# Performance work log

Measured on AMD Instinct MI355X. Metric: run time of the kernel, lower is better.

The kernel has to match this reference:

```python
import jax, jax.numpy as jnp
import numpy as np


def setup_inputs() -> dict:
    key = jax.random.key(0)
    ks = jax.random.split(key, 12)
    B, T, N, H = 32, 128, 256, 512
    s = 0.05
    return {
        "data": jax.random.normal(ks[0], (B, T, N), jnp.float32),
        "h0": jax.random.normal(ks[1], (B, H), jnp.float32),
        "gru_kernel": jax.random.normal(ks[2], (N, 3 * H), jnp.float32) * s,
        "gru_rkernel": jax.random.normal(ks[3], (H, 3 * H), jnp.float32) * s,
        "gru_bias": jax.random.normal(ks[4], (2, 3 * H), jnp.float32) * s,  # (input_bias, recurrent_bias), reset_after=True
        "w1_w": jax.random.normal(ks[5], (T, T), jnp.float32) * s,
        "w1_b": jax.random.normal(ks[6], (T,), jnp.float32) * s,
        "w2_w": jax.random.normal(ks[7], (H, T), jnp.float32) * s,
        "w2_b": jax.random.normal(ks[8], (T,), jnp.float32) * s,
        "v_w": jax.random.normal(ks[9], (T, 1), jnp.float32) * s,
        "v_b": jax.random.normal(ks[10], (1,), jnp.float32) * s,
        "n": N,
    }


def reference(data, h0, gru_kernel, gru_rkernel, gru_bias, w1_w, w1_b, w2_w, w2_b, v_w, v_b, n):
    B, T, N = data.shape
    b_in, b_rec = gru_bias[0], gru_bias[1]

    # Keras GRUCell (reset_after=True, gate order z,r,h)
    def step(h, x_t):
        mx = x_t @ gru_kernel + b_in          # (B,3H)
        mh = h @ gru_rkernel + b_rec          # (B,3H)
        xz, xr, xh = jnp.split(mx, 3, axis=-1)
        hz, hr, hh = jnp.split(mh, 3, axis=-1)
        z = jax.nn.sigmoid(xz + hz)
        r = jax.nn.sigmoid(xr + hr)
        c = jnp.tanh(xh + r * hh)
        h_new = z * h + (1.0 - z) * c
        return h_new, h_new

    xs = jnp.swapaxes(data, 0, 1)                               # (T,B,N)
    _, hs = jax.lax.scan(step, h0, xs)                          # (T,B,H) hidden state after each step

    # Input attention, vectorized over t (attention does not feed back into the GRU)
    x_perm = jnp.swapaxes(data, 1, 2)                           # (B,N,T)
    score_x = jnp.einsum('bnt,tu->bnu', x_perm, w1_w) + w1_b    # (B,N,T), constant across steps
    h_proj = hs @ w2_w + w2_b                                   # (T,B,T)
    e = jnp.tanh(score_x[None, :, :, :] + h_proj[:, :, None, :])  # (T,B,N,T)
    score = jnp.einsum('tbnu,u->tbn', e, v_w[:, 0]) + v_b[0]    # (T,B,N)
    alpha = jax.nn.softmax(score, axis=-1)                      # (T,B,N) softmax over features

    # Replicates tf.reshape(alpha_seq.stack(), (-1, T, n)) on (T,B,1,N) (row-major)
    alpha_seq = alpha.reshape(-1, T, N)                         # (B,T,N) via flat reindex, as in original
    return data * alpha_seq
```

## Files before the change

### kernel.cpp

```cpp
#include <hip/hip_runtime.h>
#include <math.h>

#define BB 32
#define TT 128
#define NF 256
#define HH 512
#define G3 1536
#define NWG 64

__device__ __forceinline__ float sigmoidf_(float x) { return 1.f / (1.f + __expf(-x)); }
__device__ __forceinline__ float tanh_fast(float x) {
    float e = __expf(2.f * x);
    return 1.f - 2.f / (e + 1.f);
}
__device__ __forceinline__ float sel4_(float a0, float a1, float a2, float a3, int s) {
    float s01 = (s & 1) ? a1 : a0;
    float s23 = (s & 1) ? a3 : a2;
    return (s & 2) ? s23 : s01;
}

__global__ __launch_bounds__(256) void k_hinit(const float* __restrict__ h0,
                                               float* __restrict__ hg2) {
    int idx = blockIdx.x * 256 + threadIdx.x;
    int i = idx & 511, b = idx >> 9;
    hg2[i * BB + b] = h0[b * HH + i];
}

__global__ __launch_bounds__(256) void k_pack(const float* __restrict__ rk,
                                              float4* __restrict__ rk4) {
    int gidx = blockIdx.x * 256 + threadIdx.x;
    int wg = gidx >> 12;
    int idx = gidx & 4095;
    int k = idx >> 3, s = idx & 7;
    int jjL = s ^ (((k >> 7) & 3) << 1);
    const float* r = rk + (size_t)k * G3 + wg * 8 + jjL;
    rk4[gidx] = make_float4(r[0], r[512], r[1024], 0.f);
}

__global__ __launch_bounds__(256) void k_mx(const float* __restrict__ data,
                                            const float* __restrict__ gk,
                                            const float* __restrict__ bias_in,
                                            float* __restrict__ mx) {
    __shared__ __align__(16) float xs[NF * 8];
    int bx = blockIdx.x;
    int t = bx >> 2, b0 = (bx & 3) * 8;
    int tid = threadIdx.x;
    for (int idx = tid; idx < 8 * NF; idx += 256) {
        int bb = idx >> 8, k = idx & 255;
        xs[k * 8 + bb] = data[((size_t)(b0 + bb) * TT + t) * NF + k];
    }
    __syncthreads();
    float acc[6][8];
#pragma unroll
    for (int jj = 0; jj < 6; jj++)
#pragma unroll
        for (int bb = 0; bb < 8; bb++) acc[jj][bb] = 0.f;

    for (int k = 0; k < NF; k++) {
        float4 xa = *(const float4*)&xs[k * 8];
        float4 xb = *(const float4*)&xs[k * 8 + 4];
        float xv[8] = {xa.x, xa.y, xa.z, xa.w, xb.x, xb.y, xb.z, xb.w};
#pragma unroll
        for (int jj = 0; jj < 6; jj++) {
            float g = gk[(size_t)k * G3 + jj * 256 + tid];
#pragma unroll
            for (int bb = 0; bb < 8; bb++) acc[jj][bb] += g * xv[bb];
        }
    }
#pragma unroll
    for (int jj = 0; jj < 6; jj++) {
        int j = jj * 256 + tid;
        float bi = bias_in[j];
#pragma unroll
        for (int bb = 0; bb < 8; bb++)
            mx[((size_t)t * BB + b0 + bb) * G3 + j] = acc[jj][bb] + bi;
    }
}

extern __shared__ float4 wl4_dyn[];

__global__ __launch_bounds__(256, 1) void k_gstep(const float4* __restrict__ rk4,
                                                  const float* __restrict__ gbias,
                                                  const float* __restrict__ mx,
                                                  float* __restrict__ hg2,
                                                  float* __restrict__ hs,
                                                  int t) {
    __shared__ __align__(16) float4 h4[HH * 8];
    const int tid = threadIdx.x;
    const int wg  = blockIdx.x;
    const int jj  = tid >> 5;
    const int bq  = (tid >> 2) & 7;
    const int ks  = tid & 3;
    const int i0  = wg * 8;
    const int i   = i0 + jj;
    const int batch = bq * 4 + ks;
    const int jjs = jj ^ (ks << 1);
    const int bqs = bq ^ (ks << 1);

    {
        const float4* src = rk4 + (size_t)wg * 4096;
#pragma unroll
        for (int it = 0; it < 16; it++) {
            int idx = it * 256 + tid;
            wl4_dyn[idx] = src[idx];
        }
    }
    {
        const float4* hgr = (const float4*)(hg2 + (t & 1) * (HH * BB));
#pragma unroll
        for (int it = 0; it < 16; it++) {
            int idx = it * 256 + tid;
            h4[idx] = hgr[idx ^ ((((idx >> 10) & 3)) << 1)];
        }
    }
    const float* brec = gbias + G3;
    const float bz = brec[i], br_ = brec[512 + i], bh = brec[1024 + i];
    __syncthreads();

    const float* mxr = mx + ((size_t)t * BB + batch) * G3;
    float mz = mxr[i], mr = mxr[512 + i], mh = mxr[1024 + i];

    float az0 = 0.f, az1 = 0.f, az2 = 0.f, az3 = 0.f;
    float ar0 = 0.f, ar1 = 0.f, ar2 = 0.f, ar3 = 0.f;
    float ah0 = 0.f, ah1 = 0.f, ah2 = 0.f, ah3 = 0.f;
    const float4* wp  = wl4_dyn + ks * 1024 + jjs;
    const float4* hp2 = &h4[ks * 1024 + bqs];
#pragma unroll 4
    for (int kk = 0; kk < 128; kk++) {
        float4 w = wp[kk * 8];
        float4 h = hp2[kk * 8];
        az0 += w.x * h.x; az1 += w.x * h.y; az2 += w.x * h.z; az3 += w.x * h.w;
        ar0 += w.y * h.x; ar1 += w.y * h.y; ar2 += w.y * h.z; ar3 += w.y * h.w;
        ah0 += w.z * h.x; ah1 += w.z * h.y; ah2 += w.z * h.z; ah3 += w.z * h.w;
    }

    az0 += __shfl_xor(az0, 1); az1 += __shfl_xor(az1, 1);
    az2 += __shfl_xor(az2, 1); az3 += __shfl_xor(az3, 1);
    ar0 += __shfl_xor(ar0, 1); ar1 += __shfl_xor(ar1, 1);
    ar2 += __shfl_xor(ar2, 1); ar3 += __shfl_xor(ar3, 1);
    ah0 += __shfl_xor(ah0, 1); ah1 += __shfl_xor(ah1, 1);
    ah2 += __shfl_xor(ah2, 1); ah3 += __shfl_xor(ah3, 1);
    az0 += __shfl_xor(az0, 2); az1 += __shfl_xor(az1, 2);
    az2 += __shfl_xor(az2, 2); az3 += __shfl_xor(az3, 2);
    ar0 += __shfl_xor(ar0, 2); ar1 += __shfl_xor(ar1, 2);
    ar2 += __shfl_xor(ar2, 2); ar3 += __shfl_xor(ar3, 2);
    ah0 += __shfl_xor(ah0, 2); ah1 += __shfl_xor(ah1, 2);
    ah2 += __shfl_xor(ah2, 2); ah3 += __shfl_xor(ah3, 2);

    float azt = sel4_(az0, az1, az2, az3, ks);
    float art = sel4_(ar0, ar1, ar2, ar3, ks);
    float aht = sel4_(ah0, ah1, ah2, ah3, ks);

    float z = sigmoidf_(mz + azt + bz);
    float r = sigmoidf_(mr + art + br_);
    float c = tanhf(mh + r * (aht + bh));
    float hold = ((const float*)&h4[i * 8 + (bq ^ ((((i >> 7) & 3)) << 1))])[ks];
    float hn = z * hold + (1.f - z) * c;

    hg2[((t + 1) & 1) * (HH * BB) + i * BB + batch] = hn;
    hs[((size_t)t * BB + batch) * HH + i] = hn;
}

__global__ __launch_bounds__(256) void k_sx(const float* __restrict__ data,
                                            const float* __restrict__ w1,
                                            const float* __restrict__ w1b,
                                            float* __restrict__ sx) {
    int bx = blockIdx.x;
    int b = bx >> 4, ug = bx & 15;
    int n = threadIdx.x;
    float acc[8] = {0, 0, 0, 0, 0, 0, 0, 0};
    const float* dp = data + (size_t)b * TT * NF + n;
    for (int t = 0; t < TT; t++) {
        float x = dp[(size_t)t * NF];
#pragma unroll
        for (int uu = 0; uu < 8; uu++) acc[uu] += x * w1[t * TT + ug * 8 + uu];
    }
#pragma unroll
    for (int uu = 0; uu < 8; uu++) {
        int u = ug * 8 + uu;
        sx[((size_t)b * TT + u) * NF + n] = acc[uu] + w1b[u];
    }
}

__global__ __launch_bounds__(256) void k_hp(const float* __restrict__ hs,
                                            const float* __restrict__ w2,
                                            const float* __restrict__ w2b,
                                            float* __restrict__ hp) {
    __shared__ float hsl[8 * HH];
    int r0 = blockIdx.x * 8;
    int tid = threadIdx.x;
    for (int idx = tid; idx < 8 * HH; idx += 256)
        hsl[idx] = hs[(size_t)r0 * HH + idx];
    __syncthreads();
    int u = tid & 127, rh = tid >> 7;
    float acc[4] = {0, 0, 0, 0};
    for (int k = 0; k < HH; k++) {
        float w = w2[k * TT + u];
#pragma unroll
        for (int rr = 0; rr < 4; rr++) acc[rr] += hsl[(rh * 4 + rr) * HH + k] * w;
    }
    float wb = w2b[u];
#pragma unroll
    for (int rr = 0; rr < 4; rr++)
        hp[(size_t)(r0 + rh * 4 + rr) * TT + u] = acc[rr] + wb;
}

__global__ __launch_bounds__(256) void k_attn(const float* __restrict__ data,
                                              const float* __restrict__ sx,
                                              const float* __restrict__ hp,
                                              const float* __restrict__ v_w,
                                              const float* __restrict__ v_b,
                                              float* __restrict__ out) {
    __shared__ float hv[TT];
    __shared__ float vv[TT];
    __shared__ float red[8];
    int r = blockIdx.x;
    int b = r & 31;
    int n = threadIdx.x;
    if (n < TT) {
        hv[n] = hp[(size_t)r * TT + n];
        vv[n] = v_w[n];
    }
    __syncthreads();
    float s = v_b[0];
    const float* sxp = sx + (size_t)b * TT * NF + n;
    for (int u = 0; u < TT; u++) {
        float e = tanh_fast(sxp[(size_t)u * NF] + hv[u]);
        s += vv[u] * e;
    }
    float m = s;
#pragma unroll
    for (int off = 32; off >= 1; off >>= 1) m = fmaxf(m, __shfl_xor(m, off));
    int lane = n & 63, wid = n >> 6;
    if (lane == 0) red[wid] = m;
    __syncthreads();
    float bm = fmaxf(fmaxf(red[0], red[1]), fmaxf(red[2], red[3]));
    float p = __expf(s - bm);
    float ps = p;
#pragma unroll
    for (int off = 32; off >= 1; off >>= 1) ps += __shfl_xor(ps, off);
    if (lane == 0) red[4 + wid] = ps;
    __syncthreads();
    float denom = red[4] + red[5] + red[6] + red[7];
    float alpha = p / denom;
    size_t idx = (size_t)r * NF + n;
    out[idx] = data[idx] * alpha;
}

extern "C" void kernel_launch(void* const* d_in, const int* in_sizes, int n_in,
                              void* d_out, int out_size, void* d_ws, size_t ws_size,
                              hipStream_t stream) {
    const float* data = (const float*)d_in[0];
    const float* h0   = (const float*)d_in[1];
    const float* gk   = (const float*)d_in[2];
    const float* rk   = (const float*)d_in[3];
    const float* gb   = (const float*)d_in[4];
    const float* w1   = (const float*)d_in[5];
    const float* w1b  = (const float*)d_in[6];
    const float* w2   = (const float*)d_in[7];
    const float* w2b  = (const float*)d_in[8];
    const float* vw   = (const float*)d_in[9];
    const float* vb   = (const float*)d_in[10];
    float* out = (float*)d_out;

    float* ws  = (float*)d_ws;
    float* mx  = ws;
    float* hs  = mx + 6291456;
    float* sxb = hs + 2097152;
    float* hp  = sxb + 1048576;
    float* hg2 = hp + 524288;
    float4* rk4 = (float4*)(hg2 + 32768);

    k_hinit<<<64, 256, 0, stream>>>(h0, hg2);
    k_pack<<<1024, 256, 0, stream>>>(rk, rk4);
    k_mx<<<512, 256, 0, stream>>>(data, gk, gb, mx);

    for (int t = 0; t < TT; t++)
        k_gstep<<<NWG, 256, 65536, stream>>>(rk4, gb, mx, hg2, hs, t);

    k_sx<<<512, 256, 0, stream>>>(data, w1, w1b, sxb);
    k_hp<<<512, 256, 0, stream>>>(hs, w2, w2b, hp);
    k_attn<<<4096, 256, 0, stream>>>(data, sxb, hp, vw, vb, out);
}
```

Baseline: 1.263 ms.

## Overlap input projection, h-projection and attention with GRU steps in one fused kernel

The separate mx, hp and attn kernels are folded into a per-step fused kernel. Extra blocks compute mx eight steps ahead, h_proj two steps behind and attention four steps behind the recurrent GRU step, so idle CUs do useful work while the latency-bound recurrence runs. The GRU blocks also load their weight and state tiles straight into LDS with global_load_lds. The cost is 132 launches instead of 128, a larger per-launch grid, and a correctness dependence on the lag distances and on stream ordering between launches.

```diff
diff --git a/kernel.cpp b/kernel.cpp
--- a/kernel.cpp
+++ b/kernel.cpp
@@ -37,13 +37,12 @@
     rk4[gidx] = make_float4(r[0], r[512], r[1024], 0.f);
 }
 
-__global__ __launch_bounds__(256) void k_mx(const float* __restrict__ data,
-                                            const float* __restrict__ gk,
-                                            const float* __restrict__ bias_in,
-                                            float* __restrict__ mx) {
-    __shared__ __align__(16) float xs[NF * 8];
-    int bx = blockIdx.x;
-    int t = bx >> 2, b0 = (bx & 3) * 8;
+__device__ __forceinline__ void mx_body(const float* __restrict__ data,
+                                        const float* __restrict__ gk,
+                                        const float* __restrict__ bias_in,
+                                        float* __restrict__ mx,
+                                        float* __restrict__ xs,
+                                        int t, int b0) {
     int tid = threadIdx.x;
     for (int idx = tid; idx < 8 * NF; idx += 256) {
         int bb = idx >> 8, k = idx & 255;
@@ -77,88 +76,13 @@
     }
 }
 
-extern __shared__ float4 wl4_dyn[];
-
-__global__ __launch_bounds__(256, 1) void k_gstep(const float4* __restrict__ rk4,
-                                                  const float* __restrict__ gbias,
-                                                  const float* __restrict__ mx,
-                                                  float* __restrict__ hg2,
-                                                  float* __restrict__ hs,
-                                                  int t) {
-    __shared__ __align__(16) float4 h4[HH * 8];
-    const int tid = threadIdx.x;
-    const int wg  = blockIdx.x;
-    const int jj  = tid >> 5;
-    const int bq  = (tid >> 2) & 7;
-    const int ks  = tid & 3;
-    const int i0  = wg * 8;
-    const int i   = i0 + jj;
-    const int batch = bq * 4 + ks;
-    const int jjs = jj ^ (ks << 1);
-    const int bqs = bq ^ (ks << 1);
-
-    {
-        const float4* src = rk4 + (size_t)wg * 4096;
-#pragma unroll
-        for (int it = 0; it < 16; it++) {
-            int idx = it * 256 + tid;
-            wl4_dyn[idx] = src[idx];
-        }
-    }
-    {
-        const float4* hgr = (const float4*)(hg2 + (t & 1) * (HH * BB));
-#pragma unroll
-        for (int it = 0; it < 16; it++) {
-            int idx = it * 256 + tid;
-            h4[idx] = hgr[idx ^ ((((idx >> 10) & 3)) << 1)];
-        }
-    }
-    const float* brec = gbias + G3;
-    const float bz = brec[i], br_ = brec[512 + i], bh = brec[1024 + i];
-    __syncthreads();
-
-    const float* mxr = mx + ((size_t)t * BB + batch) * G3;
-    float mz = mxr[i], mr = mxr[512 + i], mh = mxr[1024 + i];
-
-    float az0 = 0.f, az1 = 0.f, az2 = 0.f, az3 = 0.f;
-    float ar0 = 0.f, ar1 = 0.f, ar2 = 0.f, ar3 = 0.f;
-    float ah0 = 0.f, ah1 = 0.f, ah2 = 0.f, ah3 = 0.f;
-    const float4* wp  = wl4_dyn + ks * 1024 + jjs;
-    const float4* hp2 = &h4[ks * 1024 + bqs];
-#pragma unroll 4
-    for (int kk = 0; kk < 128; kk++) {
-        float4 w = wp[kk * 8];
-        float4 h = hp2[kk * 8];
-        az0 += w.x * h.x; az1 += w.x * h.y; az2 += w.x * h.z; az3 += w.x * h.w;
-        ar0 += w.y * h.x; ar1 += w.y * h.y; ar2 += w.y * h.z; ar3 += w.y * h.w;
-        ah0 += w.z * h.x; ah1 += w.z * h.y; ah2 += w.z * h.z; ah3 += w.z * h.w;
-    }
-
-    az0 += __shfl_xor(az0, 1); az1 += __shfl_xor(az1, 1);
-    az2 += __shfl_xor(az2, 1); az3 += __shfl_xor(az3, 1);
-    ar0 += __shfl_xor(ar0, 1); ar1 += __shfl_xor(ar1, 1);
-    ar2 += __shfl_xor(ar2, 1); ar3 += __shfl_xor(ar3, 1);
-    ah0 += __shfl_xor(ah0, 1); ah1 += __shfl_xor(ah1, 1);
-    ah2 += __shfl_xor(ah2, 1); ah3 += __shfl_xor(ah3, 1);
-    az0 += __shfl_xor(az0, 2); az1 += __shfl_xor(az1, 2);
-    az2 += __shfl_xor(az2, 2); az3 += __shfl_xor(az3, 2);
-    ar0 += __shfl_xor(ar0, 2); ar1 += __shfl_xor(ar1, 2);
-    ar2 += __shfl_xor(ar2, 2); ar3 += __shfl_xor(ar3, 2);
-    ah0 += __shfl_xor(ah0, 2); ah1 += __shfl_xor(ah1, 2);
-    ah2 += __shfl_xor(ah2, 2); ah3 += __shfl_xor(ah3, 2);
-
-    float azt = sel4_(az0, az1, az2, az3, ks);
-    float art = sel4_(ar0, ar1, ar2, ar3, ks);
-    float aht = sel4_(ah0, ah1, ah2, ah3, ks);
-
-    float z = sigmoidf_(mz + azt + bz);
-    float r = sigmoidf_(mr + art + br_);
-    float c = tanhf(mh + r * (aht + bh));
-    float hold = ((const float*)&h4[i * 8 + (bq ^ ((((i >> 7) & 3)) << 1))])[ks];
-    float hn = z * hold + (1.f - z) * c;
-
-    hg2[((t + 1) & 1) * (HH * BB) + i * BB + batch] = hn;
-    hs[((size_t)t * BB + batch) * HH + i] = hn;
+__global__ __launch_bounds__(256) void k_mx8(const float* __restrict__ data,
+                                             const float* __restrict__ gk,
+                                             const float* __restrict__ bias_in,
+                                             float* __restrict__ mx) {
+    __shared__ __align__(16) float xs[NF * 8];
+    int bx = blockIdx.x;
+    mx_body(data, gk, bias_in, mx, xs, bx >> 2, (bx & 3) * 8);
 }
 
 __global__ __launch_bounds__(256) void k_sx(const float* __restrict__ data,
@@ -182,69 +106,171 @@
     }
 }
 
-__global__ __launch_bounds__(256) void k_hp(const float* __restrict__ hs,
-                                            const float* __restrict__ w2,
-                                            const float* __restrict__ w2b,
-                                            float* __restrict__ hp) {
-    __shared__ float hsl[8 * HH];
-    int r0 = blockIdx.x * 8;
-    int tid = threadIdx.x;
-    for (int idx = tid; idx < 8 * HH; idx += 256)
-        hsl[idx] = hs[(size_t)r0 * HH + idx];
-    __syncthreads();
-    int u = tid & 127, rh = tid >> 7;
-    float acc[4] = {0, 0, 0, 0};
-    for (int k = 0; k < HH; k++) {
-        float w = w2[k * TT + u];
-#pragma unroll
-        for (int rr = 0; rr < 4; rr++) acc[rr] += hsl[(rh * 4 + rr) * HH + k] * w;
-    }
-    float wb = w2b[u];
-#pragma unroll
-    for (int rr = 0; rr < 4; rr++)
-        hp[(size_t)(r0 + rh * 4 + rr) * TT + u] = acc[rr] + wb;
-}
-
-__global__ __launch_bounds__(256) void k_attn(const float* __restrict__ data,
-                                              const float* __restrict__ sx,
-                                              const float* __restrict__ hp,
-                                              const float* __restrict__ v_w,
-                                              const float* __restrict__ v_b,
-                                              float* __restrict__ out) {
-    __shared__ float hv[TT];
-    __shared__ float vv[TT];
-    __shared__ float red[8];
-    int r = blockIdx.x;
-    int b = r & 31;
-    int n = threadIdx.x;
-    if (n < TT) {
-        hv[n] = hp[(size_t)r * TT + n];
-        vv[n] = v_w[n];
-    }
-    __syncthreads();
-    float s = v_b[0];
-    const float* sxp = sx + (size_t)b * TT * NF + n;
-    for (int u = 0; u < TT; u++) {
-        float e = tanh_fast(sxp[(size_t)u * NF] + hv[u]);
-        s += vv[u] * e;
-    }
-    float m = s;
-#pragma unroll
-    for (int off = 32; off >= 1; off >>= 1) m = fmaxf(m, __shfl_xor(m, off));
-    int lane = n & 63, wid = n >> 6;
-    if (lane == 0) red[wid] = m;
-    __syncthreads();
-    float bm = fmaxf(fmaxf(red[0], red[1]), fmaxf(red[2], red[3]));
-    float p = __expf(s - bm);
-    float ps = p;
-#pragma unroll
-    for (int off = 32; off >= 1; off >>= 1) ps += __shfl_xor(ps, off);
-    if (lane == 0) red[4 + wid] = ps;
-    __syncthreads();
-    float denom = red[4] + red[5] + red[6] + red[7];
-    float alpha = p / denom;
-    size_t idx = (size_t)r * NF + n;
-    out[idx] = data[idx] * alpha;
+extern __shared__ float4 wl4_dyn[];
+
+__global__ __launch_bounds__(256, 1) void k_fused(const float4* __restrict__ rk4,
+                                                  const float* __restrict__ gbias,
+                                                  float* __restrict__ mx,
+                                                  float* __restrict__ hg2,
+                                                  float* __restrict__ hs,
+                                                  const float* __restrict__ data,
+                                                  const float* __restrict__ gk,
+                                                  const float* __restrict__ w2,
+                                                  const float* __restrict__ w2b,
+                                                  const float* __restrict__ sxb,
+                                                  float* __restrict__ hpb,
+                                                  const float* __restrict__ v_w,
+                                                  const float* __restrict__ v_b,
+                                                  float* __restrict__ out,
+                                                  int t) {
+    __shared__ __align__(16) float4 h4[HH * 8];
+    const int bid = blockIdx.x;
+    const int tid = threadIdx.x;
+
+    if (bid < 64) {
+        if (t >= TT) return;
+        const int wg  = bid;
+        const int jj  = tid >> 5;
+        const int bq  = (tid >> 2) & 7;
+        const int ks  = tid & 3;
+        const int i0  = wg * 8;
+        const int i   = i0 + jj;
+        const int batch = bq * 4 + ks;
+        const int jjs = jj ^ (ks << 1);
+        const int bqs = bq ^ (ks << 1);
+
+        {
+            const float4* src = rk4 + (size_t)wg * 4096;
+#pragma unroll
+            for (int it = 0; it < 16; it++) {
+                int idx = it * 256 + tid;
+                __builtin_amdgcn_global_load_lds(
+                    (const __attribute__((address_space(1))) void*)(src + idx),
+                    (__attribute__((address_space(3))) void*)&wl4_dyn[idx], 16, 0, 0);
+            }
+        }
+        {
+            const float4* hgr = (const float4*)(hg2 + (t & 1) * (HH * BB));
+#pragma unroll
+            for (int it = 0; it < 16; it++) {
+                int idx = it * 256 + tid;
+                int sidx = idx ^ ((((idx >> 10) & 3)) << 1);
+                __builtin_amdgcn_global_load_lds(
+                    (const __attribute__((address_space(1))) void*)(hgr + sidx),
+                    (__attribute__((address_space(3))) void*)&h4[idx], 16, 0, 0);
+            }
+        }
+        const float* brec = gbias + G3;
+        const float bz = brec[i], br_ = brec[512 + i], bh = brec[1024 + i];
+        __syncthreads();
+
+        const float* mxr = mx + ((size_t)t * BB + batch) * G3;
+        float mz = mxr[i], mr = mxr[512 + i], mh = mxr[1024 + i];
+
+        float az0 = 0.f, az1 = 0.f, az2 = 0.f, az3 = 0.f;
+        float ar0 = 0.f, ar1 = 0.f, ar2 = 0.f, ar3 = 0.f;
+        float ah0 = 0.f, ah1 = 0.f, ah2 = 0.f, ah3 = 0.f;
+        const float4* wp  = wl4_dyn + ks * 1024 + jjs;
+        const float4* hp2 = &h4[ks * 1024 + bqs];
+#pragma unroll 4
+        for (int kk = 0; kk < 128; kk++) {
+            float4 w = wp[kk * 8];
+            float4 h = hp2[kk * 8];
+            az0 += w.x * h.x; az1 += w.x * h.y; az2 += w.x * h.z; az3 += w.x * h.w;
+            ar0 += w.y * h.x; ar1 += w.y * h.y; ar2 += w.y * h.z; ar3 += w.y * h.w;
+            ah0 += w.z * h.x; ah1 += w.z * h.y; ah2 += w.z * h.z; ah3 += w.z * h.w;
+        }
+
+        az0 += __shfl_xor(az0, 1); az1 += __shfl_xor(az1, 1);
+        az2 += __shfl_xor(az2, 1); az3 += __shfl_xor(az3, 1);
+        ar0 += __shfl_xor(ar0, 1); ar1 += __shfl_xor(ar1, 1);
+        ar2 += __shfl_xor(ar2, 1); ar3 += __shfl_xor(ar3, 1);
+        ah0 += __shfl_xor(ah0, 1); ah1 += __shfl_xor(ah1, 1);
+        ah2 += __shfl_xor(ah2, 1); ah3 += __shfl_xor(ah3, 1);
+        az0 += __shfl_xor(az0, 2); az1 += __shfl_xor(az1, 2);
+        az2 += __shfl_xor(az2, 2); az3 += __shfl_xor(az3, 2);
+        ar0 += __shfl_xor(ar0, 2); ar1 += __shfl_xor(ar1, 2);
+        ar2 += __shfl_xor(ar2, 2); ar3 += __shfl_xor(ar3, 2);
+        ah0 += __shfl_xor(ah0, 2); ah1 += __shfl_xor(ah1, 2);
+        ah2 += __shfl_xor(ah2, 2); ah3 += __shfl_xor(ah3, 2);
+
+        float azt = sel4_(az0, az1, az2, az3, ks);
+        float art = sel4_(ar0, ar1, ar2, ar3, ks);
+        float aht = sel4_(ah0, ah1, ah2, ah3, ks);
+
+        float z = sigmoidf_(mz + azt + bz);
+        float r = sigmoidf_(mr + art + br_);
+        float c = tanhf(mh + r * (aht + bh));
+        float hold = ((const float*)&h4[i * 8 + (bq ^ ((((i >> 7) & 3)) << 1))])[ks];
+        float hn = z * hold + (1.f - z) * c;
+
+        hg2[((t + 1) & 1) * (HH * BB) + i * BB + batch] = hn;
+        hs[((size_t)t * BB + batch) * HH + i] = hn;
+
+    } else if (bid < 68) {
+        int tm = t + 8;
+        if (tm >= TT) return;
+        float* xs = (float*)wl4_dyn;
+        mx_body(data, gk, gbias, mx, xs, tm, (bid - 64) * 8);
+
+    } else if (bid < 72) {
+        int th = t - 2;
+        if (th < 0 || th >= TT) return;
+        float* hsl = (float*)wl4_dyn;
+        int r0 = th * 32 + (bid - 68) * 8;
+        for (int idx = tid; idx < 8 * HH; idx += 256)
+            hsl[idx] = hs[(size_t)r0 * HH + idx];
+        __syncthreads();
+        int u = tid & 127, rh = tid >> 7;
+        float acc[4] = {0, 0, 0, 0};
+        for (int k = 0; k < HH; k++) {
+            float w = w2[k * TT + u];
+#pragma unroll
+            for (int rr = 0; rr < 4; rr++) acc[rr] += hsl[(rh * 4 + rr) * HH + k] * w;
+        }
+        float wb = w2b[u];
+#pragma unroll
+        for (int rr = 0; rr < 4; rr++)
+            hpb[(size_t)(r0 + rh * 4 + rr) * TT + u] = acc[rr] + wb;
+
+    } else {
+        int ta = t - 4;
+        if (ta < 0 || ta >= TT) return;
+        float* hv = (float*)wl4_dyn;
+        float* vv = hv + TT;
+        float* red = vv + TT;
+        int r = ta * 32 + (bid - 72);
+        int b = r & 31;
+        int n = tid;
+        if (n < TT) {
+            hv[n] = hpb[(size_t)r * TT + n];
+            vv[n] = v_w[n];
+        }
+        __syncthreads();
+        float s = v_b[0];
+        const float* sxp = sxb + (size_t)b * TT * NF + n;
+        for (int u = 0; u < TT; u++) {
+            float e = tanh_fast(sxp[(size_t)u * NF] + hv[u]);
+            s += vv[u] * e;
+        }
+        float m = s;
+#pragma unroll
+        for (int off = 32; off >= 1; off >>= 1) m = fmaxf(m, __shfl_xor(m, off));
+        int lane = n & 63, wid = n >> 6;
+        if (lane == 0) red[wid] = m;
+        __syncthreads();
+        float bm = fmaxf(fmaxf(red[0], red[1]), fmaxf(red[2], red[3]));
+        float p = __expf(s - bm);
+        float ps = p;
+#pragma unroll
+        for (int off = 32; off >= 1; off >>= 1) ps += __shfl_xor(ps, off);
+        if (lane == 0) red[4 + wid] = ps;
+        __syncthreads();
+        float denom = red[4] + red[5] + red[6] + red[7];
+        float alpha = p / denom;
+        size_t idx = (size_t)r * NF + n;
+        out[idx] = data[idx] * alpha;
+    }
 }
 
 extern "C" void kernel_launch(void* const* d_in, const int* in_sizes, int n_in,
@@ -267,18 +293,17 @@
     float* mx  = ws;
     float* hs  = mx + 6291456;
     float* sxb = hs + 2097152;
-    float* hp  = sxb + 1048576;
-    float* hg2 = hp + 524288;
+    float* hpb = sxb + 1048576;
+    float* hg2 = hpb + 524288;
     float4* rk4 = (float4*)(hg2 + 32768);
 
     k_hinit<<<64, 256, 0, stream>>>(h0, hg2);
     k_pack<<<1024, 256, 0, stream>>>(rk, rk4);
-    k_mx<<<512, 256, 0, stream>>>(data, gk, gb, mx);
-
-    for (int t = 0; t < TT; t++)
-        k_gstep<<<NWG, 256, 65536, stream>>>(rk4, gb, mx, hg2, hs, t);
-
+    k_mx8<<<32, 256, 0, stream>>>(data, gk, gb, mx);
     k_sx<<<512, 256, 0, stream>>>(data, w1, w1b, sxb);
-    k_hp<<<512, 256, 0, stream>>>(hs, w2, w2b, hp);
-    k_attn<<<4096, 256, 0, stream>>>(data, sxb, hp, vw, vb, out);
-}
+
+    for (int t = 0; t < TT + 4; t++)
+        k_fused<<<104, 256, 65536, stream>>>(rk4, gb, mx, hg2, hs,
+                                             data, gk, w2, w2b, sxb, hpb,
+                                             vw, vb, out, t);
+}
```

Result: slower. 4.053 ms (+220.8%).
